# Kernel optimization log

Measured on AMD Instinct MI355X. Metric: run time of the kernel, lower is better.

## Reference

```python
import jax, jax.numpy as jnp
import numpy as np
from jax import lax

B, S, D, H = 2, 2048, 1024, 16
DEPTH = D // H  # 64


def _leaky(x):
    # tf.keras.layers.ReLU(negative_slope=0.1)
    return jnp.where(x >= 0, x, 0.1 * x)


def _split_heads(x):
    # [B,S,D] -> [B,H,S,DEPTH]
    return x.reshape(B, S, H, DEPTH).transpose(0, 2, 1, 3)


def setup_inputs() -> dict:
    key = jax.random.key(0)
    ks = jax.random.split(key, 8)
    w = lambda k: 0.02 * jax.random.normal(k, (D, D), dtype=jnp.float32)
    return {
        "q": jax.random.normal(ks[0], (B, S, D), dtype=jnp.float32),
        "k": jax.random.normal(ks[1], (B, S, D), dtype=jnp.float32),
        "v": jax.random.normal(ks[2], (B, S, D), dtype=jnp.float32),
        "query_mask": jnp.ones((B, S, 1), dtype=jnp.float32),
        "key_mask": jnp.ones((B, S, 1), dtype=jnp.float32),
        "value_mask": jnp.ones((B, S, 1), dtype=jnp.float32),
        "Wq": w(ks[3]), "bq": 0.5 * jnp.ones((D,), dtype=jnp.float32),
        "Wk": w(ks[4]), "bk": 0.5 * jnp.ones((D,), dtype=jnp.float32),
        "Wv": w(ks[5]), "bv": jnp.zeros((D,), dtype=jnp.float32),
        "Wo": w(ks[6]), "bo": jnp.zeros((D,), dtype=jnp.float32),
    }


def _causal_linear_attn(qh, kh, vh):
    # qh,kh,vh: [B,H,S,DEPTH]. Sequential recurrence:
    #   S_t = S_{t-1} + k_t v_t^T ; z_t = z_{t-1} + k_t
    #   out_t = (q_t @ S_t) / (q_t . z_t)
    def step(carry, x):
        S_st, z = carry
        qi, ki, vi = x  # each [B,H,DEPTH]
        S_st = S_st + ki[..., :, None] * vi[..., None, :]  # [B,H,DEPTH,DEPTH]
        z = z + ki
        num = jnp.einsum('bhd,bhde->bhe', qi, S_st)
        den = jnp.einsum('bhd,bhd->bh', qi, z)
        return (S_st, z), num / den[..., None]

    init = (jnp.zeros((B, H, DEPTH, DEPTH), dtype=qh.dtype),
            jnp.zeros((B, H, DEPTH), dtype=qh.dtype))
    xs = (jnp.moveaxis(qh, 2, 0), jnp.moveaxis(kh, 2, 0), jnp.moveaxis(vh, 2, 0))
    _, out = lax.scan(step, init, xs)  # [S,B,H,DEPTH]
    return jnp.moveaxis(out, 0, 2)  # [B,H,S,DEPTH]


def reference(q, k, v, query_mask, key_mask, value_mask,
              Wq, bq, Wk, bk, Wv, bv, Wo, bo):
    q = (q * query_mask) @ Wq + bq
    k = (k * key_mask) @ Wk + bk
    v = (v * value_mask) @ Wv + bv
    q = _leaky(q)
    k = _leaky(k)
    qh, kh, vh = _split_heads(q), _split_heads(k), _split_heads(v)
    attn = _causal_linear_attn(qh, kh, vh)  # [B,H,S,DEPTH]
    concat = attn.transpose(0, 2, 1, 3).reshape(B, S, D)
    return concat @ Wo + bo
```

## Files before the change

kernel.cpp:

```cpp
#include <hip/hip_runtime.h>

#define Bx    2
#define Sx    2048
#define Dx    1024
#define Hx    16
#define NCx   (Sx/64)
#define BHx   (Bx*Hx)
#define Mx    (Bx*Sx)

typedef float    f4 __attribute__((ext_vector_type(4)));
typedef _Float16 h8 __attribute__((ext_vector_type(8)));
typedef _Float16 h4 __attribute__((ext_vector_type(4)));

__device__ __forceinline__ void gl2lds16(const _Float16* g, _Float16* l) {
  __builtin_amdgcn_global_load_lds(
      (const __attribute__((address_space(1))) void*)g,
      (__attribute__((address_space(3))) void*)l, 16, 0, 0);
}

__global__ __launch_bounds__(256) void convert_in(
    const float* __restrict__ q, const float* __restrict__ k,
    const float* __restrict__ v, const float* __restrict__ qm,
    const float* __restrict__ km, const float* __restrict__ vm,
    _Float16* __restrict__ qh, _Float16* __restrict__ kh,
    _Float16* __restrict__ vh)
{
  const int z = blockIdx.y;
  const float* x = (z == 0) ? q : (z == 1) ? k : v;
  const float* m = (z == 0) ? qm : (z == 1) ? km : vm;
  _Float16*    o = (z == 0) ? qh : (z == 1) ? kh : vh;
  const int i4 = blockIdx.x * 256 + threadIdx.x;
  const f4 vv = *(const f4*)(x + (size_t)i4 * 4);
  const float mf = m[i4 >> 8];
  h4 r;
  r[0] = (_Float16)(vv[0] * mf);
  r[1] = (_Float16)(vv[1] * mf);
  r[2] = (_Float16)(vv[2] * mf);
  r[3] = (_Float16)(vv[3] * mf);
  *(h4*)(o + (size_t)i4 * 4) = r;
}

__global__ __launch_bounds__(256) void convert_w(
    const float* __restrict__ W0, const float* __restrict__ W1,
    const float* __restrict__ W2, const float* __restrict__ W3,
    _Float16* __restrict__ T0, _Float16* __restrict__ T1,
    _Float16* __restrict__ T2, _Float16* __restrict__ T3)
{
  const float* W = (blockIdx.z == 0) ? W0 : (blockIdx.z == 1) ? W1 :
                   (blockIdx.z == 2) ? W2 : W3;
  _Float16* T = (blockIdx.z == 0) ? T0 : (blockIdx.z == 1) ? T1 :
                (blockIdx.z == 2) ? T2 : T3;
  __shared__ float Ws[64 * 68];
  const int tx = threadIdx.x & 15, ty = threadIdx.x >> 4;
  const int k0 = blockIdx.y * 64, n0 = blockIdx.x * 64;
#pragma unroll
  for (int i = 0; i < 4; i++) {
    const int r = ty + 16 * i;
    *(f4*)&Ws[r * 68 + tx * 4] = *(const f4*)&W[(size_t)(k0 + r) * Dx + n0 + tx * 4];
  }
  __syncthreads();
#pragma unroll
  for (int i = 0; i < 4; i++) {
    const int n = ty + 16 * i;
    h4 o;
#pragma unroll
    for (int j = 0; j < 4; j++) o[j] = (_Float16)Ws[(tx * 4 + j) * 68 + n];
    *(h4*)&T[(size_t)(n0 + n) * Dx + k0 + tx * 4] = o;
  }
}

struct GArgs {
  const _Float16* A; const _Float16* Bt; const float* bias;
  void* out; int leaky, half_out;
};

template<int BN, int WR, int WC>
__global__ __launch_bounds__(512, 4) void gemm_f16(GArgs g0, GArgs g1, GArgs g2)
{
  const GArgs g = (blockIdx.z == 0) ? g0 : (blockIdx.z == 1) ? g1 : g2;
  constexpr int FM = 128 / WR / 16;
  constexpr int FN = BN / WC / 16;
  __shared__ _Float16 As[128 * 64];
  __shared__ _Float16 Bs[BN * 64];
  const int tid = threadIdx.x;
  const int m0 = blockIdx.y * 128, n0 = blockIdx.x * BN;
  const int lane = tid & 63, wave = tid >> 6;
  const int lm = lane & 15, qd = lane >> 4;
  const int wr = wave % WR, wc = wave / WR;
  const int wm0 = wr * (128 / WR), wn0 = wc * (BN / WC);
  const int srow = lane >> 3;
  const int sseg = (lane & 7) ^ srow;
  const _Float16* gA = g.A  + (size_t)(m0 + srow) * Dx + sseg * 8;
  const _Float16* gB = g.Bt + (size_t)(n0 + srow) * Dx + sseg * 8;

  f4 acc[FM][FN];
#pragma unroll
  for (int i = 0; i < FM; i++)
#pragma unroll
    for (int j = 0; j < FN; j++) { f4 z = {0.f, 0.f, 0.f, 0.f}; acc[i][j] = z; }

  for (int kt = 0; kt < Dx; kt += 64) {
    __syncthreads();
#pragma unroll
    for (int u = 0; u < 2; u++) {
      const int t = wave * 2 + u;
      gl2lds16(gA + (size_t)(t * 8) * Dx + kt, &As[t * 512]);
    }
#pragma unroll
    for (int u = 0; u < BN / 64; u++) {
      const int t = wave * (BN / 64) + u;
      gl2lds16(gB + (size_t)(t * 8) * Dx + kt, &Bs[t * 512]);
    }
    __syncthreads();
#pragma unroll
    for (int kk = 0; kk < 2; kk++) {
      const int sp = ((kk * 4 + qd) ^ (lm & 7)) * 8;
      h8 af[FM];
#pragma unroll
      for (int i = 0; i < FM; i++)
        af[i] = *(const h8*)&As[(wm0 + i * 16 + lm) * 64 + sp];
#pragma unroll
      for (int j = 0; j < FN; j++) {
        const h8 bf = *(const h8*)&Bs[(wn0 + j * 16 + lm) * 64 + sp];
#pragma unroll
        for (int i = 0; i < FM; i++)
          acc[i][j] = __builtin_amdgcn_mfma_f32_16x16x32_f16(af[i], bf, acc[i][j], 0, 0, 0);
      }
    }
  }

#pragma unroll
  for (int j = 0; j < FN; j++) {
    const int n = n0 + wn0 + j * 16 + lm;
    const float bz = g.bias[n];
#pragma unroll
    for (int i = 0; i < FM; i++) {
      const int mb = m0 + wm0 + i * 16 + qd * 4;
#pragma unroll
      for (int r = 0; r < 4; r++) {
        float v = acc[i][j][r] + bz;
        if (g.leaky) v = (v >= 0.f) ? v : 0.1f * v;
        if (g.half_out) ((_Float16*)g.out)[(size_t)(mb + r) * Dx + n] = (_Float16)v;
        else            ((float*)g.out)[(size_t)(mb + r) * Dx + n] = v;
      }
    }
  }
}

__global__ __launch_bounds__(256) void chunkkv_mfma(
    const _Float16* __restrict__ kp, const _Float16* __restrict__ vp,
    _Float16* __restrict__ ckvh, float* __restrict__ cz)
{
  __shared__ _Float16 Kt[64 * 64];
  __shared__ _Float16 Vt[64 * 64];
  const int blk = blockIdx.x;
  const int c = blk & (NCx - 1);
  const int bh = blk / NCx;
  const int b = bh / Hx, h = bh % Hx;
  const int tid = threadIdx.x;
  const size_t rowbase = ((size_t)(b * Sx + c * 64)) * Dx + h * 64;

#pragma unroll
  for (int p = 0; p < 2; p++) {
    const int f = tid + 256 * p;
    const int s = f >> 3, g8 = f & 7;
    const h8 hk = *(const h8*)&kp[rowbase + (size_t)s * Dx + g8 * 8];
    const h8 hv = *(const h8*)&vp[rowbase + (size_t)s * Dx + g8 * 8];
#pragma unroll
    for (int i = 0; i < 8; i++) {
      const int r = g8 * 8 + i;
      const int a = r * 64 + (((s >> 3) ^ (r & 7)) * 8) + (s & 7);
      Kt[a] = hk[i];
      Vt[a] = hv[i];
    }
  }
  __syncthreads();

  const int lane = tid & 63, w = tid >> 6;
  const int lm = lane & 15, qd = lane >> 4;
  const int x7 = lm & 7;

  h8 av[2];
#pragma unroll
  for (int kk = 0; kk < 2; kk++)
    av[kk] = *(const h8*)&Vt[(w * 16 + lm) * 64 + (((kk << 2) + qd) ^ x7) * 8];

#pragma unroll
  for (int dt = 0; dt < 4; dt++) {
    f4 acc = {0.f, 0.f, 0.f, 0.f};
#pragma unroll
    for (int kk = 0; kk < 2; kk++) {
      const h8 bf = *(const h8*)&Kt[(dt * 16 + lm) * 64 + (((kk << 2) + qd) ^ x7) * 8];
      acc = __builtin_amdgcn_mfma_f32_16x16x32_f16(av[kk], bf, acc, 0, 0, 0);
    }
#pragma unroll
    for (int r = 0; r < 4; r++) {
      const int e = w * 16 + qd * 4 + r;
      ckvh[(size_t)blk * 4096 + e * 64 + dt * 16 + lm] = (_Float16)acc[r];
    }
  }

  {
    const int d = tid >> 2, fr = tid & 3;
    float dp = 0.f;
#pragma unroll
    for (int j = 0; j < 2; j++) {
      const h8 kv = *(const h8*)&Kt[d * 64 + (fr * 2 + j) * 8];
#pragma unroll
      for (int i = 0; i < 8; i++) dp += (float)kv[i];
    }
    dp += __shfl_xor(dp, 1);
    dp += __shfl_xor(dp, 2);
    if (fr == 0) cz[(size_t)blk * 64 + d] = dp;
  }
}

__global__ __launch_bounds__(256) void prefix_kernel(
    _Float16* __restrict__ ckvh, float* __restrict__ cz)
{
  const int gid = blockIdx.x * 256 + threadIdx.x;
  const int bh = gid >> 12, el = gid & 4095;
  float acc = 0.f;
  for (int c = 0; c < NCx; c++) {
    const size_t idx = ((size_t)(bh * NCx + c) << 12) + el;
    const float v = (float)ckvh[idx];
    ckvh[idx] = (_Float16)acc;
    acc += v;
  }
  if (gid < BHx * 64) {
    const int zbh = gid >> 6, d = gid & 63;
    float az = 0.f;
    for (int c = 0; c < NCx; c++) {
      const size_t zi = (size_t)(zbh * NCx + c) * 64 + d;
      const float v = cz[zi];
      cz[zi] = az;
      az += v;
    }
  }
}

__global__ __launch_bounds__(256) void attn_mfma(
    const _Float16* __restrict__ qp, const _Float16* __restrict__ kp,
    const _Float16* __restrict__ vp, const _Float16* __restrict__ ckvh,
    const float* __restrict__ cz, _Float16* __restrict__ concat)
{
  __shared__ _Float16 Qs[64 * 64];
  __shared__ _Float16 Ks[64 * 64];
  __shared__ _Float16 Vt[64 * 64];
  __shared__ _Float16 Sh[64 * 64];
  __shared__ float zs[64];
  __shared__ float den[64];
  const int blk = blockIdx.x;
  const int c = blk & (NCx - 1);
  const int bh = blk / NCx;
  const int b = bh / Hx, h = bh % Hx;
  const int tid = threadIdx.x;
  const size_t rowbase = ((size_t)(b * Sx + c * 64)) * Dx + h * 64;

#pragma unroll
  for (int p = 0; p < 2; p++) {
    const int f = tid + 256 * p;
    const int r = f >> 3, sg = f & 7;
    const int ph = (sg ^ (r & 7)) * 8;
    *(h8*)&Qs[r * 64 + ph] = *(const h8*)&qp[rowbase + (size_t)r * Dx + sg * 8];
    *(h8*)&Ks[r * 64 + ph] = *(const h8*)&kp[rowbase + (size_t)r * Dx + sg * 8];
    *(h8*)&Sh[r * 64 + ph] = *(const h8*)&ckvh[(size_t)blk * 4096 + r * 64 + sg * 8];
  }
#pragma unroll
  for (int p = 0; p < 2; p++) {
    const int f = tid + 256 * p;
    const int s = f >> 3, g8 = f & 7;
    const h8 hv = *(const h8*)&vp[rowbase + (size_t)s * Dx + g8 * 8];
#pragma unroll
    for (int i = 0; i < 8; i++) {
      const int e = g8 * 8 + i;
      Vt[e * 64 + (((s >> 3) ^ (e & 7)) * 8) + (s & 7)] = hv[i];
    }
  }
  if (tid < 64) zs[tid] = cz[(size_t)blk * 64 + tid];
  __syncthreads();

  const int lane = tid & 63, w = tid >> 6;
  const int lm = lane & 15, qd = lane >> 4;
  const int x7 = lm & 7;

  h8 aq[2];
#pragma unroll
  for (int kk = 0; kk < 2; kk++)
    aq[kk] = *(const h8*)&Qs[(w * 16 + lm) * 64 + (((kk << 2) + qd) ^ x7) * 8];

  f4 pc[4];
#pragma unroll
  for (int st = 0; st < 4; st++) {
    f4 z4 = {0.f, 0.f, 0.f, 0.f}; pc[st] = z4;
#pragma unroll
    for (int kk = 0; kk < 2; kk++) {
      const h8 bf = *(const h8*)&Ks[(st * 16 + lm) * 64 + (((kk << 2) + qd) ^ x7) * 8];
      pc[st] = __builtin_amdgcn_mfma_f32_16x16x32_f16(aq[kk], bf, pc[st], 0, 0, 0);
    }
  }
  float rsum[4] = {0.f, 0.f, 0.f, 0.f};
#pragma unroll
  for (int st = 0; st < 4; st++) {
    const int s = st * 16 + lm;
#pragma unroll
    for (int r = 0; r < 4; r++) {
      const int t = w * 16 + qd * 4 + r;
      float v = pc[st][r];
      v = (s <= t) ? v : 0.f;
      pc[st][r] = v;
      rsum[r] += v;
    }
  }
#pragma unroll
  for (int r = 0; r < 4; r++) {
    rsum[r] += __shfl_xor(rsum[r], 1);
    rsum[r] += __shfl_xor(rsum[r], 2);
    rsum[r] += __shfl_xor(rsum[r], 4);
    rsum[r] += __shfl_xor(rsum[r], 8);
  }
  {
    const int t = tid >> 2, fr = tid & 3;
    float dp = 0.f;
#pragma unroll
    for (int j = 0; j < 2; j++) {
      const int sg = fr * 2 + j;
      const h8 qv = *(const h8*)&Qs[t * 64 + (sg ^ (t & 7)) * 8];
#pragma unroll
      for (int i = 0; i < 8; i++) dp += (float)qv[i] * zs[sg * 8 + i];
    }
    dp += __shfl_xor(dp, 1);
    dp += __shfl_xor(dp, 2);
    if (fr == 0) den[t] = dp;
  }
  __syncthreads();

  _Float16* Pa = Ks;
#pragma unroll
  for (int st = 0; st < 4; st++) {
#pragma unroll
    for (int r = 0; r < 4; r++) {
      const int row = w * 16 + qd * 4 + r;
      Pa[row * 64 + (((st * 2 + (lm >> 3)) ^ (row & 7)) * 8) + (lm & 7)] =
          (_Float16)pc[st][r];
    }
  }
  if (lm == 0) {
#pragma unroll
    for (int r = 0; r < 4; r++) den[w * 16 + qd * 4 + r] += rsum[r];
  }
  __syncthreads();

  h8 ap[2];
#pragma unroll
  for (int kk = 0; kk < 2; kk++)
    ap[kk] = *(const h8*)&Pa[(w * 16 + lm) * 64 + (((kk << 2) + qd) ^ x7) * 8];

  f4 acc[4];
#pragma unroll
  for (int et = 0; et < 4; et++) {
    f4 z4 = {0.f, 0.f, 0.f, 0.f}; acc[et] = z4;
#pragma unroll
    for (int kk = 0; kk < 2; kk++) {
      const h8 bv = *(const h8*)&Vt[(et * 16 + lm) * 64 + (((kk << 2) + qd) ^ x7) * 8];
      acc[et] = __builtin_amdgcn_mfma_f32_16x16x32_f16(ap[kk], bv, acc[et], 0, 0, 0);
    }
#pragma unroll
    for (int kk = 0; kk < 2; kk++) {
      const h8 bs = *(const h8*)&Sh[(et * 16 + lm) * 64 + (((kk << 2) + qd) ^ x7) * 8];
      acc[et] = __builtin_amdgcn_mfma_f32_16x16x32_f16(aq[kk], bs, acc[et], 0, 0, 0);
    }
  }

#pragma unroll
  for (int r = 0; r < 4; r++) {
    const int row = w * 16 + qd * 4 + r;
    const float inv = 1.f / den[row];
    _Float16* orow = &concat[((size_t)(b * Sx + c * 64 + row)) * Dx + h * 64];
#pragma unroll
    for (int et = 0; et < 4; et++)
      orow[et * 16 + lm] = (_Float16)(acc[et][r] * inv);
  }
}

extern "C" void kernel_launch(void* const* d_in, const int* in_sizes, int n_in,
                              void* d_out, int out_size, void* d_ws, size_t ws_size,
                              hipStream_t stream)
{
  const float* q  = (const float*)d_in[0];
  const float* k  = (const float*)d_in[1];
  const float* v  = (const float*)d_in[2];
  const float* qm = (const float*)d_in[3];
  const float* km = (const float*)d_in[4];
  const float* vm = (const float*)d_in[5];
  const float* Wq = (const float*)d_in[6];
  const float* bq = (const float*)d_in[7];
  const float* Wk = (const float*)d_in[8];
  const float* bk = (const float*)d_in[9];
  const float* Wv = (const float*)d_in[10];
  const float* bv = (const float*)d_in[11];
  const float* Wo = (const float*)d_in[12];
  const float* bo = (const float*)d_in[13];
  float* out = (float*)d_out;

  char* ws = (char*)d_ws;
  _Float16* qh  = (_Float16*)(ws);
  _Float16* kh  = (_Float16*)(ws + 8388608);
  _Float16* vh  = (_Float16*)(ws + 16777216);
  _Float16* Wtq = (_Float16*)(ws + 25165824);
  _Float16* Wtk = (_Float16*)(ws + 27262976);
  _Float16* Wtv = (_Float16*)(ws + 29360128);
  _Float16* Wto = (_Float16*)(ws + 31457280);
  _Float16* qp  = (_Float16*)(ws + 33554432);
  _Float16* kp  = (_Float16*)(ws + 41943040);
  _Float16* vp  = (_Float16*)(ws + 50331648);
  float*    cz  = (float*)   (ws + 58720256);
  _Float16* ckvh   = qh;
  _Float16* concat = kh;

  convert_in<<<dim3(4096, 3), 256, 0, stream>>>(q, k, v, qm, km, vm, qh, kh, vh);
  convert_w<<<dim3(16, 16, 4), 256, 0, stream>>>(Wq, Wk, Wv, Wo, Wtq, Wtk, Wtv, Wto);

  GArgs gq = { qh, Wtq, bq, qp, 1, 1 };
  GArgs gk = { kh, Wtk, bk, kp, 1, 1 };
  GArgs gv = { vh, Wtv, bv, vp, 0, 1 };
  gemm_f16<128, 4, 2><<<dim3(Dx / 128, Mx / 128, 3), 512, 0, stream>>>(gq, gk, gv);

  chunkkv_mfma<<<BHx * NCx, 256, 0, stream>>>(kp, vp, ckvh, cz);
  prefix_kernel<<<512, 256, 0, stream>>>(ckvh, cz);
  attn_mfma<<<BHx * NCx, 256, 0, stream>>>(qp, kp, vp, ckvh, cz, concat);

  GArgs go = { concat, Wto, bo, out, 0, 0 };
  gemm_f16<64, 4, 2><<<dim3(Dx / 64, Mx / 128, 1), 512, 0, stream>>>(go, go, go);
}
```

Measured before the change: 203.8 us.

## Fuse fp32 input masking and fp16 conversion into QKV GEMM A-tile loads

New measurement: 212.8 us. 1.04x slower.

```diff
diff --git a/kernel.cpp b/kernel.cpp
--- a/kernel.cpp
+++ b/kernel.cpp
@@ -18,28 +18,6 @@
       (__attribute__((address_space(3))) void*)l, 16, 0, 0);
 }
 
-__global__ __launch_bounds__(256) void convert_in(
-    const float* __restrict__ q, const float* __restrict__ k,
-    const float* __restrict__ v, const float* __restrict__ qm,
-    const float* __restrict__ km, const float* __restrict__ vm,
-    _Float16* __restrict__ qh, _Float16* __restrict__ kh,
-    _Float16* __restrict__ vh)
-{
-  const int z = blockIdx.y;
-  const float* x = (z == 0) ? q : (z == 1) ? k : v;
-  const float* m = (z == 0) ? qm : (z == 1) ? km : vm;
-  _Float16*    o = (z == 0) ? qh : (z == 1) ? kh : vh;
-  const int i4 = blockIdx.x * 256 + threadIdx.x;
-  const f4 vv = *(const f4*)(x + (size_t)i4 * 4);
-  const float mf = m[i4 >> 8];
-  h4 r;
-  r[0] = (_Float16)(vv[0] * mf);
-  r[1] = (_Float16)(vv[1] * mf);
-  r[2] = (_Float16)(vv[2] * mf);
-  r[3] = (_Float16)(vv[3] * mf);
-  *(h4*)(o + (size_t)i4 * 4) = r;
-}
-
 __global__ __launch_bounds__(256) void convert_w(
     const float* __restrict__ W0, const float* __restrict__ W1,
     const float* __restrict__ W2, const float* __restrict__ W3,
@@ -70,11 +48,11 @@
 }
 
 struct GArgs {
-  const _Float16* A; const _Float16* Bt; const float* bias;
+  const void* A; const _Float16* Bt; const float* bias; const float* mask;
   void* out; int leaky, half_out;
 };
 
-template<int BN, int WR, int WC>
+template<int BN, int WR, int WC, int A32>
 __global__ __launch_bounds__(512, 4) void gemm_f16(GArgs g0, GArgs g1, GArgs g2)
 {
   const GArgs g = (blockIdx.z == 0) ? g0 : (blockIdx.z == 1) ? g1 : g2;
@@ -90,8 +68,21 @@
   const int wm0 = wr * (128 / WR), wn0 = wc * (BN / WC);
   const int srow = lane >> 3;
   const int sseg = (lane & 7) ^ srow;
-  const _Float16* gA = g.A  + (size_t)(m0 + srow) * Dx + sseg * 8;
   const _Float16* gB = g.Bt + (size_t)(n0 + srow) * Dx + sseg * 8;
+
+  const _Float16* gA16 = nullptr;
+  const float* gA32[2];
+  float mf[2];
+  if (A32) {
+#pragma unroll
+    for (int u = 0; u < 2; u++) {
+      const int r = m0 + (wave * 2 + u) * 8 + srow;
+      gA32[u] = (const float*)g.A + (size_t)r * Dx + sseg * 8;
+      mf[u] = g.mask[r];
+    }
+  } else {
+    gA16 = (const _Float16*)g.A + (size_t)(m0 + srow) * Dx + sseg * 8;
+  }
 
   f4 acc[FM][FN];
 #pragma unroll
@@ -101,10 +92,25 @@
 
   for (int kt = 0; kt < Dx; kt += 64) {
     __syncthreads();
-#pragma unroll
-    for (int u = 0; u < 2; u++) {
-      const int t = wave * 2 + u;
-      gl2lds16(gA + (size_t)(t * 8) * Dx + kt, &As[t * 512]);
+    if (A32) {
+#pragma unroll
+      for (int u = 0; u < 2; u++) {
+        const f4 a0 = *(const f4*)(gA32[u] + kt);
+        const f4 a1 = *(const f4*)(gA32[u] + kt + 4);
+        h8 o;
+#pragma unroll
+        for (int i = 0; i < 4; i++) {
+          o[i]     = (_Float16)(a0[i] * mf[u]);
+          o[4 + i] = (_Float16)(a1[i] * mf[u]);
+        }
+        *(h8*)&As[(wave * 2 + u) * 512 + lane * 8] = o;
+      }
+    } else {
+#pragma unroll
+      for (int u = 0; u < 2; u++) {
+        const int t = wave * 2 + u;
+        gl2lds16(gA16 + (size_t)(t * 8) * Dx + kt, &As[t * 512]);
+      }
     }
 #pragma unroll
     for (int u = 0; u < BN / 64; u++) {
@@ -220,22 +226,29 @@
 {
   const int gid = blockIdx.x * 256 + threadIdx.x;
   const int bh = gid >> 12, el = gid & 4095;
+  const size_t base = (((size_t)bh * NCx) << 12) + el;
+  float vals[NCx];
+#pragma unroll
+  for (int c = 0; c < NCx; c++)
+    vals[c] = (float)ckvh[base + ((size_t)c << 12)];
   float acc = 0.f;
-  for (int c = 0; c < NCx; c++) {
-    const size_t idx = ((size_t)(bh * NCx + c) << 12) + el;
-    const float v = (float)ckvh[idx];
-    ckvh[idx] = (_Float16)acc;
-    acc += v;
-  }
+#pragma unroll
+  for (int c = 0; c < NCx; c++) { const float t = vals[c]; vals[c] = acc; acc += t; }
+#pragma unroll
+  for (int c = 0; c < NCx; c++)
+    ckvh[base + ((size_t)c << 12)] = (_Float16)vals[c];
+
   if (gid < BHx * 64) {
     const int zbh = gid >> 6, d = gid & 63;
+    const size_t zb = (size_t)zbh * NCx * 64 + d;
+    float zv[NCx];
+#pragma unroll
+    for (int c = 0; c < NCx; c++) zv[c] = cz[zb + (size_t)c * 64];
     float az = 0.f;
-    for (int c = 0; c < NCx; c++) {
-      const size_t zi = (size_t)(zbh * NCx + c) * 64 + d;
-      const float v = cz[zi];
-      cz[zi] = az;
-      az += v;
-    }
+#pragma unroll
+    for (int c = 0; c < NCx; c++) { const float t = zv[c]; zv[c] = az; az += t; }
+#pragma unroll
+    for (int c = 0; c < NCx; c++) cz[zb + (size_t)c * 64] = zv[c];
   }
 }
 
@@ -404,9 +417,8 @@
   float* out = (float*)d_out;
 
   char* ws = (char*)d_ws;
-  _Float16* qh  = (_Float16*)(ws);
-  _Float16* kh  = (_Float16*)(ws + 8388608);
-  _Float16* vh  = (_Float16*)(ws + 16777216);
+  _Float16* ckvh   = (_Float16*)(ws);
+  _Float16* concat = (_Float16*)(ws + 8388608);
   _Float16* Wtq = (_Float16*)(ws + 25165824);
   _Float16* Wtk = (_Float16*)(ws + 27262976);
   _Float16* Wtv = (_Float16*)(ws + 29360128);
@@ -415,21 +427,18 @@
   _Float16* kp  = (_Float16*)(ws + 41943040);
   _Float16* vp  = (_Float16*)(ws + 50331648);
   float*    cz  = (float*)   (ws + 58720256);
-  _Float16* ckvh   = qh;
-  _Float16* concat = kh;
-
-  convert_in<<<dim3(4096, 3), 256, 0, stream>>>(q, k, v, qm, km, vm, qh, kh, vh);
+
   convert_w<<<dim3(16, 16, 4), 256, 0, stream>>>(Wq, Wk, Wv, Wo, Wtq, Wtk, Wtv, Wto);
 
-  GArgs gq = { qh, Wtq, bq, qp, 1, 1 };
-  GArgs gk = { kh, Wtk, bk, kp, 1, 1 };
-  GArgs gv = { vh, Wtv, bv, vp, 0, 1 };
-  gemm_f16<128, 4, 2><<<dim3(Dx / 128, Mx / 128, 3), 512, 0, stream>>>(gq, gk, gv);
+  GArgs gq = { q, Wtq, bq, qm, qp, 1, 1 };
+  GArgs gk = { k, Wtk, bk, km, kp, 1, 1 };
+  GArgs gv = { v, Wtv, bv, vm, vp, 0, 1 };
+  gemm_f16<128, 4, 2, 1><<<dim3(Dx / 128, Mx / 128, 3), 512, 0, stream>>>(gq, gk, gv);
 
   chunkkv_mfma<<<BHx * NCx, 256, 0, stream>>>(kp, vp, ckvh, cz);
   prefix_kernel<<<512, 256, 0, stream>>>(ckvh, cz);
   attn_mfma<<<BHx * NCx, 256, 0, stream>>>(qp, kp, vp, ckvh, cz, concat);
 
-  GArgs go = { concat, Wto, bo, out, 0, 0 };
-  gemm_f16<64, 4, 2><<<dim3(Dx / 64, Mx / 128, 1), 512, 0, stream>>>(go, go, go);
-}
+  GArgs go = { concat, Wto, bo, nullptr, out, 0, 0 };
+  gemm_f16<64, 4, 2, 0><<<dim3(Dx / 64, Mx / 128, 1), 512, 0, stream>>>(go, go, go);
+}
```
